# Kernel tuning notes

Hardware: AMD Instinct MI355X
Metric: run time of the kernel (lower is better)

## Reference

```python
import jax, jax.numpy as jnp
import numpy as np

I, H, O = 32, 64, 8  # input_size, hidden_layer, output_size
B, T = 4096, 256


def setup_inputs() -> dict:
    key = jax.random.key(0)
    ks = jax.random.split(key, 7)
    s_ih = 1.0 / np.sqrt(H)
    return {
        "x": jax.random.normal(ks[0], (B, T, I), dtype=jnp.float32),
        # PyTorch nn.LSTM params, gate order [i, f, g, o]
        "W_ih": jax.random.uniform(ks[1], (4 * H, I), jnp.float32, -s_ih, s_ih),
        "W_hh": jax.random.uniform(ks[2], (4 * H, H), jnp.float32, -s_ih, s_ih),
        "b_ih": jax.random.uniform(ks[3], (4 * H,), jnp.float32, -s_ih, s_ih),
        "b_hh": jax.random.uniform(ks[4], (4 * H,), jnp.float32, -s_ih, s_ih),
        "W_fc": jax.random.uniform(ks[5], (O, H), jnp.float32, -s_ih, s_ih),
        "b_fc": jax.random.uniform(ks[6], (O,), jnp.float32, -s_ih, s_ih),
    }


def reference(x, W_ih, W_hh, b_ih, b_hh, W_fc, b_fc):
    # Precompute input-to-hidden projections for all timesteps in one GEMM.
    # [B, T, 4H]
    x_proj = jnp.einsum('bti,gi->btg', x, W_ih) + b_ih + b_hh

    def step(carry, xp_t):
        h, c = carry  # [B, H] each
        gates = xp_t + h @ W_hh.T  # [B, 4H]
        i_g, f_g, g_g, o_g = jnp.split(gates, 4, axis=-1)
        i_g = jax.nn.sigmoid(i_g)
        f_g = jax.nn.sigmoid(f_g)
        g_g = jnp.tanh(g_g)
        o_g = jax.nn.sigmoid(o_g)
        c = f_g * c + i_g * g_g
        h = o_g * jnp.tanh(c)
        return (h, c), None

    h0 = jnp.zeros((x.shape[0], H), dtype=x.dtype)
    c0 = jnp.zeros((x.shape[0], H), dtype=x.dtype)
    # scan over time axis: move T to leading axis
    (h_T, c_T), _ = jax.lax.scan(step, (h0, c0), jnp.swapaxes(x_proj, 0, 1))
    # out[:, -1, :] == final hidden state for single-layer batch_first LSTM
    return h_T @ W_fc.T + b_fc
```

## Files before the change

### kernel.cpp

```cpp
#include <hip/hip_runtime.h>
#include <hip/hip_bf16.h>


#define T_LEN 256
#define I_SZ  32
#define H_SZ  64
#define O_SZ  8
#define BR    8
#define HS    72

typedef __attribute__((ext_vector_type(8))) short short8;
typedef __attribute__((ext_vector_type(4))) float f32x4;
typedef __attribute__((ext_vector_type(2))) float f32x2;

static __device__ __forceinline__ unsigned fbits(float f) {
    union { float f; unsigned u; } v; v.f = f; return v.u;
}
static __device__ __forceinline__ unsigned pk2t(float lo, float hi) {
    return __builtin_amdgcn_perm(fbits(hi), fbits(lo), 0x07060302u);
}
static __device__ __forceinline__ short f2bf_rne(float f) {
    union { __hip_bfloat16 b; short s; } u;
    u.b = __float2bfloat16(f);
    return u.s;
}

#define LOG2E     1.4426950408889634f
#define TWO_LOG2E 2.8853900817779268f

static __device__ __forceinline__ f32x2 sig2(f32x2 x) {
    float ex = __builtin_amdgcn_exp2f(x.x * (-LOG2E));
    float ey = __builtin_amdgcn_exp2f(x.y * (-LOG2E));
    f32x2 r;
    r.x = __builtin_amdgcn_rcpf(ex + 1.0f);
    r.y = __builtin_amdgcn_rcpf(ey + 1.0f);
    return r;
}
static __device__ __forceinline__ f32x2 tanh2(f32x2 x) {
    float cx = __builtin_amdgcn_fmed3f(x.x, -10.0f, 10.0f);
    float cy = __builtin_amdgcn_fmed3f(x.y, -10.0f, 10.0f);
    float ex = __builtin_amdgcn_exp2f(cx * TWO_LOG2E);
    float ey = __builtin_amdgcn_exp2f(cy * TWO_LOG2E);
    f32x2 r;
    r.x = (ex - 1.0f) * __builtin_amdgcn_rcpf(ex + 1.0f);
    r.y = (ey - 1.0f) * __builtin_amdgcn_rcpf(ey + 1.0f);
    return r;
}
static __device__ __forceinline__ f32x2 fma2(f32x2 a, f32x2 b, f32x2 c) {
    return __builtin_elementwise_fma(a, b, c);
}

__global__ __launch_bounds__(256, 2)
void lstm_fused_kernel(const float* __restrict__ x,
                       const float* __restrict__ W_ih,
                       const float* __restrict__ W_hh,
                       const float* __restrict__ b_ih,
                       const float* __restrict__ b_hh,
                       const float* __restrict__ W_fc,
                       const float* __restrict__ b_fc,
                       float* __restrict__ out)
{
    __shared__ short hbuf[2][8][HS];
    __shared__ float Hf[BR][64];

    const int tid  = threadIdx.x;
    const int wave = tid >> 6;
    const int lane = tid & 63;
    const int quad = lane >> 4;
    const int nlow = lane & 15;
    const int jw   = wave * 16 + nlow;
    const int b0   = blockIdx.x * BR;

    const int fr = (nlow < 8) ? nlow : (((nlow & 4) ? 6 : 2) + (nlow & 1));
    const int ra = ((quad & 1) << 2) | (quad & 2);

    short8 bfrag[4][3];
    f32x4  biasf[4];
    for (int g = 0; g < 4; ++g) {
        const int col = g * 64 + jw;
        {
            const float* wr = W_ih + col * I_SZ + quad * 8;
            short8 f;
            #pragma unroll
            for (int e = 0; e < 8; ++e) f[e] = f2bf_rne(wr[e]);
            bfrag[g][0] = f;
        }
        #pragma unroll
        for (int kt = 1; kt < 3; ++kt) {
            const float* wr = W_hh + col * H_SZ + (kt - 1) * 32 + quad * 8;
            short8 f;
            #pragma unroll
            for (int e = 0; e < 8; ++e) f[e] = f2bf_rne(wr[e]);
            bfrag[g][kt] = f;
        }
        const float bg = b_ih[col] + b_hh[col];
        biasf[g] = (f32x4){bg, bg, bg, bg};
    }

    for (int q = tid; q < 2 * 8 * HS; q += 256) ((short*)hbuf)[q] = (short)0;

    const float* xb = x + ((size_t)(b0 + fr) * T_LEN) * I_SZ + quad * 8;

    float4 nx[16];
    short8 sc[8];
    #pragma unroll
    for (int s = 0; s < 8; ++s) {
        nx[2*s]   = *(const float4*)(xb + s * I_SZ);
        nx[2*s+1] = *(const float4*)(xb + s * I_SZ + 4);
    }
    #pragma unroll
    for (int s = 0; s < 8; ++s) {
        union { uint4 u; short8 v; } w;
        w.u.x = pk2t(nx[2*s].x,   nx[2*s].y);
        w.u.y = pk2t(nx[2*s].z,   nx[2*s].w);
        w.u.z = pk2t(nx[2*s+1].x, nx[2*s+1].y);
        w.u.w = pk2t(nx[2*s+1].z, nx[2*s+1].w);
        sc[s] = w.v;
    }

    const short* rb[2] = { &hbuf[0][fr][quad * 8], &hbuf[1][fr][quad * 8] };
    short*       wb[2] = { &hbuf[0][ra][jw],       &hbuf[1][ra][jw] };

    f32x2 cc = {0.f, 0.f};
    f32x2 hh = {0.f, 0.f};

    for (int ch = 0; ch < 32; ++ch) {
        #pragma unroll
        for (int tc = 0; tc < 8; ++tc) {
            const int t = ch * 8 + tc;

            __syncthreads();

            const short* hr = rb[t & 1];
            short8 a1 = *(const short8*)(hr);
            short8 a2 = *(const short8*)(hr + 32);

            if (tc == 0 && ch + 1 < 32) {
                const float* nxt = xb + (t + 8) * I_SZ;
                #pragma unroll
                for (int s = 0; s < 8; ++s) {
                    nx[2*s]   = *(const float4*)(nxt + s * I_SZ);
                    nx[2*s+1] = *(const float4*)(nxt + s * I_SZ + 4);
                }
            }

            const short8 ax = sc[tc];

            f32x4 acc[4];
            #pragma unroll
            for (int g = 0; g < 4; ++g) {
                f32x4 a = __builtin_amdgcn_mfma_f32_16x16x32_bf16(ax, bfrag[g][0], biasf[g], 0, 0, 0);
                a = __builtin_amdgcn_mfma_f32_16x16x32_bf16(a1, bfrag[g][1], a, 0, 0, 0);
                a = __builtin_amdgcn_mfma_f32_16x16x32_bf16(a2, bfrag[g][2], a, 0, 0, 0);
                acc[g] = a;
            }

            if (tc == 7 && ch + 1 < 32) {
                #pragma unroll
                for (int s = 0; s < 8; ++s) {
                    union { uint4 u; short8 v; } w;
                    w.u.x = pk2t(nx[2*s].x,   nx[2*s].y);
                    w.u.y = pk2t(nx[2*s].z,   nx[2*s].w);
                    w.u.z = pk2t(nx[2*s+1].x, nx[2*s+1].y);
                    w.u.w = pk2t(nx[2*s+1].z, nx[2*s+1].w);
                    sc[s] = w.v;
                }
            }

            f32x2 pI = {acc[0][0], acc[0][1]};
            f32x2 pF = {acc[1][0], acc[1][1]};
            f32x2 pG = {acc[2][0], acc[2][1]};
            f32x2 pO = {acc[3][0], acc[3][1]};

            f32x2 iv = sig2(pI);
            f32x2 fv = sig2(pF);
            f32x2 gv = tanh2(pG);
            f32x2 ov = sig2(pO);
            cc = fma2(fv, cc, iv * gv);
            hh = ov * tanh2(cc);

            short* hw = wb[(t + 1) & 1];
            hw[0]  = (short)((fbits(hh.x) + 0x8000u) >> 16);
            hw[HS] = (short)((fbits(hh.y) + 0x8000u) >> 16);
        }
    }

    Hf[ra][jw]     = hh.x;
    Hf[ra + 1][jw] = hh.y;
    __syncthreads();

    if (tid < BR * O_SZ) {
        const int r = tid >> 3;
        const int o = tid & 7;
        const float* wf = W_fc + o * H_SZ;
        float acc = b_fc[o];
        #pragma unroll
        for (int jx = 0; jx < H_SZ; ++jx) acc += Hf[r][jx] * wf[jx];
        out[(size_t)(b0 + r) * O_SZ + o] = acc;
    }
}

extern "C" void kernel_launch(void* const* d_in, const int* in_sizes, int n_in,
                              void* d_out, int out_size, void* d_ws, size_t ws_size,
                              hipStream_t stream) {
    const float* x    = (const float*)d_in[0];
    const float* W_ih = (const float*)d_in[1];
    const float* W_hh = (const float*)d_in[2];
    const float* b_ih = (const float*)d_in[3];
    const float* b_hh = (const float*)d_in[4];
    const float* W_fc = (const float*)d_in[5];
    const float* b_fc = (const float*)d_in[6];
    float* out = (float*)d_out;

    const int B = 4096;
    lstm_fused_kernel<<<dim3(B / BR), dim3(256), 0, stream>>>(
        x, W_ih, W_hh, b_ih, b_hh, W_fc, b_fc, out);
}
```

Baseline: 305.6 us.

## Hoist input-projection MFMA off recurrent path and fuse gate reciprocals

Measured after the change: 297.9 us. 2.5% less time.

```diff
diff --git a/kernel.cpp b/kernel.cpp
--- a/kernel.cpp
+++ b/kernel.cpp
@@ -24,31 +24,34 @@
     u.b = __float2bfloat16(f);
     return u.s;
 }
+static __device__ __forceinline__ f32x2 rcp2(f32x2 d) {
+    f32x2 r;
+    r.x = __builtin_amdgcn_rcpf(d.x);
+    r.y = __builtin_amdgcn_rcpf(d.y);
+    return r;
+}
+static __device__ __forceinline__ f32x2 exp2_2(f32x2 m) {
+    f32x2 e;
+    e.x = __builtin_amdgcn_exp2f(m.x);
+    e.y = __builtin_amdgcn_exp2f(m.y);
+    return e;
+}
+static __device__ __forceinline__ f32x2 clamp2(f32x2 x, float lo, float hi) {
+    f32x2 r;
+    r.x = __builtin_amdgcn_fmed3f(x.x, lo, hi);
+    r.y = __builtin_amdgcn_fmed3f(x.y, lo, hi);
+    return r;
+}
+static __device__ __forceinline__ f32x2 fma2(f32x2 a, f32x2 b, f32x2 c) {
+    return __builtin_elementwise_fma(a, b, c);
+}
+static __device__ __forceinline__ void lds_barrier() {
+    asm volatile("s_waitcnt lgkmcnt(0)\n\ts_barrier" ::: "memory");
+}
 
 #define LOG2E     1.4426950408889634f
 #define TWO_LOG2E 2.8853900817779268f
-
-static __device__ __forceinline__ f32x2 sig2(f32x2 x) {
-    float ex = __builtin_amdgcn_exp2f(x.x * (-LOG2E));
-    float ey = __builtin_amdgcn_exp2f(x.y * (-LOG2E));
-    f32x2 r;
-    r.x = __builtin_amdgcn_rcpf(ex + 1.0f);
-    r.y = __builtin_amdgcn_rcpf(ey + 1.0f);
-    return r;
-}
-static __device__ __forceinline__ f32x2 tanh2(f32x2 x) {
-    float cx = __builtin_amdgcn_fmed3f(x.x, -10.0f, 10.0f);
-    float cy = __builtin_amdgcn_fmed3f(x.y, -10.0f, 10.0f);
-    float ex = __builtin_amdgcn_exp2f(cx * TWO_LOG2E);
-    float ey = __builtin_amdgcn_exp2f(cy * TWO_LOG2E);
-    f32x2 r;
-    r.x = (ex - 1.0f) * __builtin_amdgcn_rcpf(ex + 1.0f);
-    r.y = (ey - 1.0f) * __builtin_amdgcn_rcpf(ey + 1.0f);
-    return r;
-}
-static __device__ __forceinline__ f32x2 fma2(f32x2 a, f32x2 b, f32x2 c) {
-    return __builtin_elementwise_fma(a, b, c);
-}
+#define ECLAMP    28.8f
 
 __global__ __launch_bounds__(256, 2)
 void lstm_fused_kernel(const float* __restrict__ x,
@@ -77,12 +80,13 @@
     short8 bfrag[4][3];
     f32x4  biasf[4];
     for (int g = 0; g < 4; ++g) {
+        const float scale = (g == 2) ? -TWO_LOG2E : -LOG2E;
         const int col = g * 64 + jw;
         {
             const float* wr = W_ih + col * I_SZ + quad * 8;
             short8 f;
             #pragma unroll
-            for (int e = 0; e < 8; ++e) f[e] = f2bf_rne(wr[e]);
+            for (int e = 0; e < 8; ++e) f[e] = f2bf_rne(scale * wr[e]);
             bfrag[g][0] = f;
         }
         #pragma unroll
@@ -90,10 +94,10 @@
             const float* wr = W_hh + col * H_SZ + (kt - 1) * 32 + quad * 8;
             short8 f;
             #pragma unroll
-            for (int e = 0; e < 8; ++e) f[e] = f2bf_rne(wr[e]);
+            for (int e = 0; e < 8; ++e) f[e] = f2bf_rne(scale * wr[e]);
             bfrag[g][kt] = f;
         }
-        const float bg = b_ih[col] + b_hh[col];
+        const float bg = scale * (b_ih[col] + b_hh[col]);
         biasf[g] = (f32x4){bg, bg, bg, bg};
     }
 
@@ -124,12 +128,22 @@
     f32x2 cc = {0.f, 0.f};
     f32x2 hh = {0.f, 0.f};
 
+    f32x4 preacc[4];
+    #pragma unroll
+    for (int g = 0; g < 4; ++g)
+        preacc[g] = __builtin_amdgcn_mfma_f32_16x16x32_bf16(sc[0], bfrag[g][0], biasf[g], 0, 0, 0);
+
+    {
+        const int dly = (blockIdx.x ^ (blockIdx.x >> 3) ^ (blockIdx.x >> 6)) & 7;
+        for (int i = 0; i < dly; ++i) asm volatile("s_sleep 1");
+    }
+
     for (int ch = 0; ch < 32; ++ch) {
         #pragma unroll
         for (int tc = 0; tc < 8; ++tc) {
             const int t = ch * 8 + tc;
 
-            __syncthreads();
+            lds_barrier();
 
             const short* hr = rb[t & 1];
             short8 a1 = *(const short8*)(hr);
@@ -144,13 +158,10 @@
                 }
             }
 
-            const short8 ax = sc[tc];
-
             f32x4 acc[4];
             #pragma unroll
             for (int g = 0; g < 4; ++g) {
-                f32x4 a = __builtin_amdgcn_mfma_f32_16x16x32_bf16(ax, bfrag[g][0], biasf[g], 0, 0, 0);
-                a = __builtin_amdgcn_mfma_f32_16x16x32_bf16(a1, bfrag[g][1], a, 0, 0, 0);
+                f32x4 a = __builtin_amdgcn_mfma_f32_16x16x32_bf16(a1, bfrag[g][1], preacc[g], 0, 0, 0);
                 a = __builtin_amdgcn_mfma_f32_16x16x32_bf16(a2, bfrag[g][2], a, 0, 0, 0);
                 acc[g] = a;
             }
@@ -167,17 +178,25 @@
                 }
             }
 
-            f32x2 pI = {acc[0][0], acc[0][1]};
-            f32x2 pF = {acc[1][0], acc[1][1]};
-            f32x2 pG = {acc[2][0], acc[2][1]};
-            f32x2 pO = {acc[3][0], acc[3][1]};
-
-            f32x2 iv = sig2(pI);
-            f32x2 fv = sig2(pF);
-            f32x2 gv = tanh2(pG);
-            f32x2 ov = sig2(pO);
-            cc = fma2(fv, cc, iv * gv);
-            hh = ov * tanh2(cc);
+            const short8 nax = sc[(tc + 1) & 7];
+            #pragma unroll
+            for (int g = 0; g < 4; ++g)
+                preacc[g] = __builtin_amdgcn_mfma_f32_16x16x32_bf16(nax, bfrag[g][0], biasf[g], 0, 0, 0);
+
+            f32x2 pi = {acc[0][0], acc[0][1]};
+            f32x2 pf = {acc[1][0], acc[1][1]};
+            f32x2 pg = {acc[2][0], acc[2][1]};
+            f32x2 po = {acc[3][0], acc[3][1]};
+
+            f32x2 ei = exp2_2(pi);
+            f32x2 ef = exp2_2(pf);
+            f32x2 eg = exp2_2(clamp2(pg, -ECLAMP, ECLAMP));
+            f32x2 eo = exp2_2(po);
+            f32x2 fv = rcp2(ef + 1.0f);
+            f32x2 ig = (1.0f - eg) * rcp2((ei + 1.0f) * (eg + 1.0f));
+            cc = fma2(fv, cc, ig);
+            f32x2 ec = exp2_2(clamp2(cc * (-TWO_LOG2E), -ECLAMP, ECLAMP));
+            hh = (1.0f - ec) * rcp2((eo + 1.0f) * (ec + 1.0f));
 
             short* hw = wb[(t + 1) & 1];
             hw[0]  = (short)((fbits(hh.x) + 0x8000u) >> 16);
```
